# Kernel tuning notes

Measured on AMD Instinct MI355X. Metric: run time of the kernel, lower is better.

The kernel has to match this reference:

```python
import jax, jax.numpy as jnp
from jax import lax
import numpy as np

ROI = 7  # roi_size


def _extract_rois(feat, coords):
    """Faithful port of extract_roi_features: clamp a 7x7 window to image bounds,
    then bilinearly resize the (possibly smaller) crop back to 7x7
    (F.interpolate, mode='bilinear', align_corners=False)."""
    B, C, H, W = feat.shape
    half = ROI // 2

    def axis_idx(c, size):
        start = jnp.maximum(0, c - half)                  # [B,A]
        end = jnp.minimum(size, c + half + 1)
        Li = end - start                                  # crop length (int) [B,A]
        L = Li.astype(feat.dtype)[..., None]              # [B,A,1]
        j = jnp.arange(ROI, dtype=feat.dtype)
        # align_corners=False source coordinate, clamped into the crop
        src = jnp.clip((j + 0.5) * L / ROI - 0.5, 0.0, L - 1.0)  # [B,A,7]
        i0 = jnp.floor(src).astype(jnp.int32)
        i1 = jnp.minimum(i0 + 1, Li[..., None] - 1)
        w1 = src - i0.astype(feat.dtype)
        return start[..., None] + i0, start[..., None] + i1, 1.0 - w1, w1

    xc = coords[..., 0].astype(jnp.int32)
    yc = coords[..., 1].astype(jnp.int32)
    y0, y1, wy0, wy1 = axis_idx(yc, H)
    x0, x1, wx0, wx1 = axis_idx(xc, W)
    Bn, A = xc.shape
    bi = jnp.arange(Bn)[:, None, None, None]

    def g(Y, X):  # gather -> [B,A,7,7,C]
        return feat[bi, :, Y[:, :, :, None], X[:, :, None, :]]

    wy0 = wy0[:, :, :, None, None]; wy1 = wy1[:, :, :, None, None]
    wx0 = wx0[:, :, None, :, None]; wx1 = wx1[:, :, None, :, None]
    v = (wy0 * wx0 * g(y0, x0) + wy0 * wx1 * g(y0, x1)
         + wy1 * wx0 * g(y1, x0) + wy1 * wx1 * g(y1, x1))
    return jnp.transpose(v, (0, 1, 4, 2, 3))  # [B,A,C,7,7]


def _conv(x, w, b, pad):
    y = lax.conv_general_dilated(x, w, (1, 1), [(pad, pad), (pad, pad)],
                                 dimension_numbers=('NCHW', 'OIHW', 'NCHW'))
    return y + b[None, :, None, None]


def _bn(x, scale, bias, mean, var, eps=1e-5):
    inv = scale * lax.rsqrt(var + eps)
    return x * inv[None, :, None, None] + (bias - mean * inv)[None, :, None, None]


def setup_inputs() -> dict:
    key = jax.random.key(0)
    ks = jax.random.split(key, 12)
    B, A, C, H, W = 8, 128, 256, 64, 64
    f32 = jnp.float32
    d = {}
    d['feat_rgb'] = jax.random.normal(ks[0], (B, C, H, W), f32)
    d['feat_tir'] = jax.random.normal(ks[1], (B, C, H, W), f32)
    d['anchor_coords'] = jax.random.randint(ks[2], (B, A, 2), 0, 64).astype(jnp.int32)
    # local_fusion: Conv(2C->C,3) BN ReLU Conv(C->C,3) BN ReLU
    d['conv1_w'] = jax.random.normal(ks[3], (C, 2 * C, 3, 3), f32) * 0.02
    d['conv1_b'] = jnp.zeros((C,), f32)
    d['bn1_scale'] = jnp.ones((C,), f32)
    d['bn1_bias'] = jnp.zeros((C,), f32)
    d['bn1_mean'] = jax.random.normal(ks[4], (C,), f32) * 0.1
    d['bn1_var'] = jax.random.uniform(ks[5], (C,), f32, 0.5, 1.5)
    d['conv2_w'] = jax.random.normal(ks[6], (C, C, 3, 3), f32) * 0.02
    d['conv2_b'] = jnp.zeros((C,), f32)
    d['bn2_scale'] = jnp.ones((C,), f32)
    d['bn2_bias'] = jnp.zeros((C,), f32)
    d['bn2_mean'] = jax.random.normal(ks[7], (C,), f32) * 0.1
    d['bn2_var'] = jax.random.uniform(ks[8], (C,), f32, 0.5, 1.5)
    # weight_generator: Conv(C->C//4,1) ReLU Conv(C//4->2,1) Softmax(dim=1)
    d['wg1_w'] = jax.random.normal(ks[9], (C // 4, C, 1, 1), f32) * 0.05
    d['wg1_b'] = jnp.zeros((C // 4,), f32)
    d['wg2_w'] = jax.random.normal(ks[10], (2, C // 4, 1, 1), f32) * 0.05
    d['wg2_b'] = jnp.zeros((2,), f32)
    return d


def reference(feat_rgb, feat_tir, anchor_coords,
              conv1_w, conv1_b, bn1_scale, bn1_bias, bn1_mean, bn1_var,
              conv2_w, conv2_b, bn2_scale, bn2_bias, bn2_mean, bn2_var,
              wg1_w, wg1_b, wg2_w, wg2_b):
    B, C, H, W = feat_rgb.shape
    A = anchor_coords.shape[1]
    roi_rgb = _extract_rois(feat_rgb, anchor_coords)  # [B,A,C,7,7]
    roi_tir = _extract_rois(feat_tir, anchor_coords)
    rgb = roi_rgb.reshape(B * A, C, ROI, ROI)
    tir = roi_tir.reshape(B * A, C, ROI, ROI)
    x = jnp.concatenate([rgb, tir], axis=1)           # [B*A, 2C, 7, 7]
    x = jax.nn.relu(_bn(_conv(x, conv1_w, conv1_b, 1), bn1_scale, bn1_bias, bn1_mean, bn1_var))
    x = jax.nn.relu(_bn(_conv(x, conv2_w, conv2_b, 1), bn2_scale, bn2_bias, bn2_mean, bn2_var))
    h = jax.nn.relu(_conv(x, wg1_w, wg1_b, 0))
    w = jax.nn.softmax(_conv(h, wg2_w, wg2_b, 0), axis=1)  # [B*A, 2, 7, 7]
    fused = w[:, 0:1] * rgb + w[:, 1:2] * tir
    return fused.reshape(B, A, C, ROI, ROI)
```

## Files before the change

### kernel.cpp

```cpp
#include <hip/hip_runtime.h>
#include <cstddef>
#include <cstdint>


typedef unsigned int u32;
typedef unsigned short u16;
typedef __attribute__((ext_vector_type(8))) short short8;
typedef __attribute__((ext_vector_type(16))) float float16v;

__device__ __forceinline__ float bf2f(u16 u) {
  u32 x = ((u32)u) << 16;
  return __builtin_bit_cast(float, x);
}
__device__ __forceinline__ u16 f2bf(float f) {
  u32 x = __builtin_bit_cast(u32, f);
  x = x + 0x7fffu + ((x >> 16) & 1u);
  return (u16)(x >> 16);
}
__device__ __forceinline__ void gl_lds16(const void* g, void* l) {
  __builtin_amdgcn_global_load_lds((const __attribute__((address_space(1))) void*)g,
                                   (__attribute__((address_space(3))) void*)l, 16, 0, 0);
}

template <int IC>
__global__ void k_prep_w(const float* __restrict__ w, u16* __restrict__ wt) {
  int i = blockIdx.x * 256 + threadIdx.x;
  if (i >= 9 * 256 * IC) return;
  int e = i & 7;
  int r = i >> 3;
  int oc = r & 255;
  int r2 = r >> 8;
  int oct = r2 % (IC / 8);
  int t = r2 / (IC / 8);
  int ic = oct * 8 + e;
  wt[i] = f2bf(w[((size_t)oc * IC + ic) * 9 + t]);
}

__global__ void k_prep_bn(const float* __restrict__ cb, const float* __restrict__ sc,
                          const float* __restrict__ bi, const float* __restrict__ mn,
                          const float* __restrict__ vr, float* __restrict__ sb) {
  int c = threadIdx.x;
  float inv = sc[c] * rsqrtf(vr[c] + 1e-5f);
  sb[c]       = inv;
  sb[256 + c] = cb[c] * inv + (bi[c] - mn[c] * inv);
}

__global__ __launch_bounds__(256)
void k_roi2(const float* __restrict__ frgb, const float* __restrict__ ftir,
            const int* __restrict__ coords, u16* __restrict__ cat) {
  int ba = blockIdx.x, b = ba >> 7, tid = threadIdx.x;
  __shared__ int   si0[2][7], si1[2][7];
  __shared__ float sw0[2][7], sw1[2][7];
  __shared__ u16 tile[49][514];
  if (tid < 14) {
    int axis = tid / 7;
    int j = tid - axis * 7;
    int c = coords[ba * 2 + (axis == 0 ? 1 : 0)];
    int start = max(0, c - 3);
    int end   = min(64, c + 4);
    int Li = end - start;
    float L = (float)Li;
    float src = ((float)j + 0.5f) * L / 7.0f - 0.5f;
    src = fminf(fmaxf(src, 0.0f), L - 1.0f);
    int i0 = (int)floorf(src);
    int i1 = min(i0 + 1, Li - 1);
    float w1 = src - (float)i0;
    si0[axis][j] = start + i0;
    si1[axis][j] = start + i1;
    sw0[axis][j] = 1.0f - w1;
    sw1[axis][j] = w1;
  }
  __syncthreads();
  const float* fr = frgb + (size_t)b * 256 * 4096;
  const float* ft = ftir + (size_t)b * 256 * 4096;
  for (int idx = tid; idx < 256 * 49; idx += 256) {
    int c = idx / 49, p = idx - c * 49;
    int jy = p / 7, jx = p - (p / 7) * 7;
    int y0 = si0[0][jy], y1 = si1[0][jy];
    int x0 = si0[1][jx], x1 = si1[1][jx];
    float wy0 = sw0[0][jy], wy1 = sw1[0][jy];
    float wx0 = sw0[1][jx], wx1 = sw1[1][jx];
    float a00 = wy0 * wx0, a01 = wy0 * wx1, a10 = wy1 * wx0, a11 = wy1 * wx1;
    const float* fc = fr + (size_t)c * 4096;
    float vr_ = a00 * fc[y0 * 64 + x0] + a01 * fc[y0 * 64 + x1] +
                a10 * fc[y1 * 64 + x0] + a11 * fc[y1 * 64 + x1];
    const float* gc = ft + (size_t)c * 4096;
    float vt_ = a00 * gc[y0 * 64 + x0] + a01 * gc[y0 * 64 + x1] +
                a10 * gc[y1 * 64 + x0] + a11 * gc[y1 * 64 + x1];
    tile[p][c]       = f2bf(vr_);
    tile[p][256 + c] = f2bf(vt_);
  }
  __syncthreads();
  u16* dst = cat + (size_t)ba * 49 * 512;
  for (int o = tid; o < 49 * 512; o += 256) {
    int row = o >> 9, c = o & 511;
    dst[o] = tile[row][c];
  }
}

template <int ICT, bool FIRST>
__global__ __launch_bounds__(512, 4)
void k_conv_mfma(const u16* __restrict__ IN, const u16* __restrict__ WT,
                 const float* __restrict__ sb, u16* __restrict__ OUT) {
  constexpr int NC = ICT / 64;
  constexpr int ROIB = 137 * 128;
  constexpr int BUFB = 2 * ROIB;
  __shared__ __align__(16) u16 lds[2][BUFB / 2];
  const int tid = threadIdx.x;
  const int lane = tid & 63, wv = tid >> 6;
  const int ng = wv & 3, mg = wv >> 2;
  const int l31 = lane & 31, h32 = lane >> 5;
  const int ba2 = blockIdx.x * 2;
  const char* inb = (const char*)IN;

  {
    short8 zz = (short8){0, 0, 0, 0, 0, 0, 0, 0};
    short8* lp = (short8*)&lds[0][0];
    for (int z = tid; z < (2 * BUFB) / 16; z += 512) lp[z] = zz;
  }
  __syncthreads();

  int rg[2];
#pragma unroll
  for (int i = 0; i < 2; ++i) {
    int P = (mg * 2 + i) * 32 + l31;
    if (P > 97) P = 97;
    int roi = (P >= 49) ? 1 : 0;
    int q = P - roi * 49;
    int qy = q / 7, qx = q - (q / 7) * 7;
    rg[i] = roi * 137 + qy * 16 + qx;
  }

  float16v acc[2][2];
#pragma unroll
  for (int i = 0; i < 2; ++i)
#pragma unroll
    for (int f = 0; f < 2; ++f)
#pragma unroll
      for (int e = 0; e < 16; ++e) acc[i][f][e] = 0.0f;

  auto stage = [&](int ch, int buf) {
    for (int s = wv; s < 14; s += 8) {
      int roi = s / 7, qy = s - roi * 7;
      char* dbase = (char*)&lds[buf][0] + roi * ROIB + ((qy + 1) * 16 + 1) * 128;
      if (lane < 56) {
        int r = roi * 137 + (qy + 1) * 16 + 1 + (lane >> 3);
        int cl = ((lane & 7) * 16) ^ ((r & 7) << 4);
        const char* src = inb +
            ((size_t)((ba2 + roi) * 49 + qy * 7 + (lane >> 3))) * (ICT * 2) +
            ch * 128 + cl;
        gl_lds16(src, dbase);
      }
    }
  };

  stage(0, 0);
  __syncthreads();

  const u16* wthr = WT + (size_t)h32 * 2048 + (size_t)(ng * 64 + l31) * 8;

  int cur = 0;
#pragma unroll 1
  for (int ch = 0; ch < NC; ++ch) {
    if (ch + 1 < NC) stage(ch + 1, cur ^ 1);
    const char* lb = (const char*)&lds[cur][0];
    const u16* wch = wthr + (size_t)ch * 8 * 2048;

    short8 wfr[4][2];
#pragma unroll
    for (int jp = 0; jp < 3; ++jp)
#pragma unroll
      for (int f = 0; f < 2; ++f)
        wfr[jp][f] = *(const short8*)(
            wch + (size_t)(jp * 2) * 2048 + f * 256);
#pragma unroll
    for (int j = 0; j < 36; ++j) {
      if (j + 3 < 36) {
        const int jn = j + 3;
#pragma unroll
        for (int f = 0; f < 2; ++f)
          wfr[jn & 3][f] = *(const short8*)(
              wch + (size_t)((jn >> 2) * (ICT / 8) + (jn & 3) * 2) * 2048 + f * 256);
      }
      const int t = j >> 2, kk = j & 3;
      const int toff = (t / 3) * 16 + (t - (t / 3) * 3);
      short8 bfr[2];
#pragma unroll
      for (int i = 0; i < 2; ++i) {
        int r = rg[i] + toff;
        int byt = r * 128 + ((kk * 32 + h32 * 16) ^ ((r & 7) << 4));
        bfr[i] = *(const short8*)(lb + byt);
      }
      __builtin_amdgcn_s_setprio(1);
#pragma unroll
      for (int i = 0; i < 2; ++i)
#pragma unroll
        for (int f = 0; f < 2; ++f)
          acc[i][f] = FIRST
              ? __builtin_amdgcn_mfma_f32_32x32x16_bf16(bfr[i], wfr[j & 3][f],
                                                        acc[i][f], 0, 0, 0)
              : __builtin_amdgcn_mfma_f32_32x32x16_bf16(wfr[j & 3][f], bfr[i],
                                                        acc[i][f], 0, 0, 0);
      __builtin_amdgcn_s_setprio(0);
    }
    __syncthreads();
    cur ^= 1;
  }

  if (FIRST) {
    u16* ob = OUT + (size_t)ba2 * 49 * 256;
#pragma unroll
    for (int f = 0; f < 2; ++f) {
      int oc = ng * 64 + f * 32 + l31;
      float s = sb[oc], bb = sb[256 + oc];
#pragma unroll
      for (int i = 0; i < 2; ++i) {
        int tl = mg * 2 + i;
#pragma unroll
        for (int reg = 0; reg < 16; ++reg) {
          int m = (reg & 3) + 8 * (reg >> 2) + 4 * h32;
          int P = tl * 32 + m;
          if (P < 98) {
            int roi = (P >= 49) ? 1 : 0;
            int q = P - roi * 49;
            ob[((size_t)roi * 49 + q) * 256 + oc] =
                f2bf(fmaxf(acc[i][f][reg] * s + bb, 0.0f));
          }
        }
      }
    }
  } else {
    u16* ob = OUT + (size_t)ba2 * 256 * 49;
#pragma unroll
    for (int i = 0; i < 2; ++i) {
      int tl = mg * 2 + i;
      int P = tl * 32 + l31;
      if (P < 98) {
        int roi = (P >= 49) ? 1 : 0;
        int q = P - roi * 49;
#pragma unroll
        for (int f = 0; f < 2; ++f)
#pragma unroll
          for (int reg = 0; reg < 16; ++reg) {
            int oc = ng * 64 + f * 32 + (reg & 3) + 8 * (reg >> 2) + 4 * h32;
            float s = sb[oc], bb = sb[256 + oc];
            ob[((size_t)roi * 256 + oc) * 49 + q] =
                f2bf(fmaxf(acc[i][f][reg] * s + bb, 0.0f));
          }
      }
    }
  }
}

__global__ __launch_bounds__(256)
void k_head_fuse(const u16* __restrict__ x3, const u16* __restrict__ cat,
                 const float* __restrict__ w1, const float* __restrict__ b1,
                 const float* __restrict__ w2, const float* __restrict__ b2,
                 float* __restrict__ out) {
  int ba  = blockIdx.x;
  int tid = threadIdx.x;
  __shared__ float xs[256 * 49];
  __shared__ float hs[64 * 49];
  __shared__ float ls[2 * 49];
  __shared__ float swx[2 * 49];
  const u16* src = x3 + (size_t)ba * 256 * 49;
  for (int idx = tid; idx < 256 * 49; idx += 256) xs[idx] = bf2f(src[idx]);
  __syncthreads();
  for (int idx = tid; idx < 64 * 49; idx += 256) {
    int oh = idx / 49, p = idx - oh * 49;
    float s = b1[oh];
    const float* wr = w1 + oh * 256;
    for (int ic = 0; ic < 256; ++ic) s += wr[ic] * xs[ic * 49 + p];
    hs[idx] = fmaxf(s, 0.0f);
  }
  __syncthreads();
  if (tid < 98) {
    int chn = tid / 49, p = tid - chn * 49;
    float s = b2[chn];
    const float* wr = w2 + chn * 64;
    for (int k = 0; k < 64; ++k) s += wr[k] * hs[k * 49 + p];
    ls[tid] = s;
  }
  __syncthreads();
  if (tid < 49) {
    float l0 = ls[tid], l1 = ls[49 + tid];
    float m = fmaxf(l0, l1);
    float e0 = expf(l0 - m), e1 = expf(l1 - m);
    float d = e0 + e1;
    swx[tid]      = e0 / d;
    swx[49 + tid] = e1 / d;
  }
  __syncthreads();
  const u16* cr = cat + (size_t)ba * 49 * 512;
  float* o = out + (size_t)ba * 256 * 49;
  for (int idx = tid; idx < 256 * 49; idx += 256) {
    int c = idx / 49, p = idx - (idx / 49) * 49;
    float rgb = bf2f(cr[p * 512 + c]);
    float tir = bf2f(cr[p * 512 + 256 + c]);
    o[idx] = swx[p] * rgb + swx[49 + p] * tir;
  }
}

extern "C" void kernel_launch(void* const* d_in, const int* in_sizes, int n_in,
                              void* d_out, int out_size, void* d_ws, size_t ws_size,
                              hipStream_t stream) {
  const float* feat_rgb = (const float*)d_in[0];
  const float* feat_tir = (const float*)d_in[1];
  const int*   coords   = (const int*)d_in[2];
  const float* conv1_w  = (const float*)d_in[3];
  const float* conv1_b  = (const float*)d_in[4];
  const float* bn1_s    = (const float*)d_in[5];
  const float* bn1_b    = (const float*)d_in[6];
  const float* bn1_m    = (const float*)d_in[7];
  const float* bn1_v    = (const float*)d_in[8];
  const float* conv2_w  = (const float*)d_in[9];
  const float* conv2_b  = (const float*)d_in[10];
  const float* bn2_s    = (const float*)d_in[11];
  const float* bn2_b    = (const float*)d_in[12];
  const float* bn2_m    = (const float*)d_in[13];
  const float* bn2_v    = (const float*)d_in[14];
  const float* wg1_w    = (const float*)d_in[15];
  const float* wg1_b    = (const float*)d_in[16];
  const float* wg2_w    = (const float*)d_in[17];
  const float* wg2_b    = (const float*)d_in[18];
  float* out = (float*)d_out;

  char* base = (char*)d_ws;
  u16*   W1T  = (u16*)(base);
  u16*   W2T  = (u16*)(base + 2359296);
  float* SB1  = (float*)(base + 2359296 + 1179648);
  float* SB2  = (float*)(base + 2359296 + 1179648 + 2048);
  u16*   CAT  = (u16*)(base + 3543040);
  u16*   X2   = (u16*)(base + 3543040 + 51380224);
  u16*   X3   = (u16*)(base + 3543040 + 51380224 + 25690112);

  k_prep_w<512><<<(9 * 256 * 512 + 255) / 256, 256, 0, stream>>>(conv1_w, W1T);
  k_prep_w<256><<<(9 * 256 * 256 + 255) / 256, 256, 0, stream>>>(conv2_w, W2T);
  k_prep_bn<<<1, 256, 0, stream>>>(conv1_b, bn1_s, bn1_b, bn1_m, bn1_v, SB1);
  k_prep_bn<<<1, 256, 0, stream>>>(conv2_b, bn2_s, bn2_b, bn2_m, bn2_v, SB2);
  k_roi2<<<1024, 256, 0, stream>>>(feat_rgb, feat_tir, coords, CAT);
  k_conv_mfma<512, true><<<512, 512, 0, stream>>>(CAT, W1T, SB1, X2);
  k_conv_mfma<256, false><<<512, 512, 0, stream>>>(X2, W2T, SB2, X3);
  k_head_fuse<<<1024, 256, 0, stream>>>(X3, CAT, wg1_w, wg1_b, wg2_w, wg2_b, out);
}
```

Measured before the change: 640.2 us.

## Prefetch LDS operand fragments, change swizzle, and use non-temporal LDS loads

The conv MFMA loop now double-buffers the LDS activation fragments, loading iteration j+1 before issuing the MFMAs for j. To balance register use, weight-fragment prefetch depth drops from 3 to 2 buffers. The LDS XOR swizzle now mixes in higher row bits (r ^ r>>4) to reduce bank conflicts, and the global-to-LDS loads use a non-temporal cache policy. Together these aim to hide LDS latency behind the MFMAs. The shallower weight prefetch and the changed cache hint could expose global-load latency.

```diff
diff --git a/kernel.cpp b/kernel.cpp
--- a/kernel.cpp
+++ b/kernel.cpp
@@ -17,9 +17,9 @@
   x = x + 0x7fffu + ((x >> 16) & 1u);
   return (u16)(x >> 16);
 }
-__device__ __forceinline__ void gl_lds16(const void* g, void* l) {
+__device__ __forceinline__ void gl_lds16_nt(const void* g, void* l) {
   __builtin_amdgcn_global_load_lds((const __attribute__((address_space(1))) void*)g,
-                                   (__attribute__((address_space(3))) void*)l, 16, 0, 0);
+                                   (__attribute__((address_space(3))) void*)l, 16, 0, 2);
 }
 
 template <int IC>
@@ -145,11 +145,12 @@
       char* dbase = (char*)&lds[buf][0] + roi * ROIB + ((qy + 1) * 16 + 1) * 128;
       if (lane < 56) {
         int r = roi * 137 + (qy + 1) * 16 + 1 + (lane >> 3);
-        int cl = ((lane & 7) * 16) ^ ((r & 7) << 4);
+        int sw = ((r ^ (r >> 4)) & 7) << 4;
+        int cl = ((lane & 7) * 16) ^ sw;
         const char* src = inb +
             ((size_t)((ba2 + roi) * 49 + qy * 7 + (lane >> 3))) * (ICT * 2) +
             ch * 128 + cl;
-        gl_lds16(src, dbase);
+        gl_lds16_nt(src, dbase);
       }
     }
   };
@@ -166,30 +167,40 @@
     const char* lb = (const char*)&lds[cur][0];
     const u16* wch = wthr + (size_t)ch * 8 * 2048;
 
-    short8 wfr[4][2];
-#pragma unroll
-    for (int jp = 0; jp < 3; ++jp)
+    short8 wfr[3][2];
+#pragma unroll
+    for (int jp = 0; jp < 2; ++jp)
 #pragma unroll
       for (int f = 0; f < 2; ++f)
         wfr[jp][f] = *(const short8*)(
             wch + (size_t)(jp * 2) * 2048 + f * 256);
+    short8 bfr[2][2];
+#pragma unroll
+    for (int i = 0; i < 2; ++i) {
+      int r = rg[i];
+      int byt = r * 128 + ((h32 * 16) ^ (((r ^ (r >> 4)) & 7) << 4));
+      bfr[0][i] = *(const short8*)(lb + byt);
+    }
 #pragma unroll
     for (int j = 0; j < 36; ++j) {
-      if (j + 3 < 36) {
-        const int jn = j + 3;
+      if (j + 2 < 36) {
+        const int jn = j + 2;
 #pragma unroll
         for (int f = 0; f < 2; ++f)
-          wfr[jn & 3][f] = *(const short8*)(
+          wfr[jn % 3][f] = *(const short8*)(
               wch + (size_t)((jn >> 2) * (ICT / 8) + (jn & 3) * 2) * 2048 + f * 256);
       }
-      const int t = j >> 2, kk = j & 3;
-      const int toff = (t / 3) * 16 + (t - (t / 3) * 3);
-      short8 bfr[2];
-#pragma unroll
-      for (int i = 0; i < 2; ++i) {
-        int r = rg[i] + toff;
-        int byt = r * 128 + ((kk * 32 + h32 * 16) ^ ((r & 7) << 4));
-        bfr[i] = *(const short8*)(lb + byt);
+      if (j + 1 < 36) {
+        const int jn = j + 1;
+        const int t2 = jn >> 2, kk2 = jn & 3;
+        const int toff2 = (t2 / 3) * 16 + (t2 - (t2 / 3) * 3);
+#pragma unroll
+        for (int i = 0; i < 2; ++i) {
+          int r = rg[i] + toff2;
+          int byt = r * 128 +
+                    ((kk2 * 32 + h32 * 16) ^ (((r ^ (r >> 4)) & 7) << 4));
+          bfr[jn & 1][i] = *(const short8*)(lb + byt);
+        }
       }
       __builtin_amdgcn_s_setprio(1);
 #pragma unroll
@@ -197,9 +208,9 @@
 #pragma unroll
         for (int f = 0; f < 2; ++f)
           acc[i][f] = FIRST
-              ? __builtin_amdgcn_mfma_f32_32x32x16_bf16(bfr[i], wfr[j & 3][f],
+              ? __builtin_amdgcn_mfma_f32_32x32x16_bf16(bfr[j & 1][i], wfr[j % 3][f],
                                                         acc[i][f], 0, 0, 0)
-              : __builtin_amdgcn_mfma_f32_32x32x16_bf16(wfr[j & 3][f], bfr[i],
+              : __builtin_amdgcn_mfma_f32_32x32x16_bf16(wfr[j % 3][f], bfr[j & 1][i],
                                                         acc[i][f], 0, 0, 0);
       __builtin_amdgcn_s_setprio(0);
     }
```

Result: no change. 632.2 us (-1.3%).

## Process four ROIs per conv block with 1024 threads and compact LDS layout

Applied to the files above, without the earlier changes.

The conv kernel now handles four ROIs per block using 16 waves, so each weight fragment loaded from global memory is reused across twice as many output positions. The padded 16-wide LDS halo layout is replaced by a compact 196-row layout plus one zero row. Out-of-bounds 3x3 taps are redirected to that zero row with a per-tap bounds check, which shrinks staging and LDS zero-fill. Padding waste drops from 128 to 98 positions per ROI pair, with one idle wave group handled via a dead flag. The cost is index arithmetic per tap, fewer blocks (256) for the GPU's many CUs, and higher register pressure at 1024 threads.

```diff
diff --git a/kernel.cpp b/kernel.cpp
--- a/kernel.cpp
+++ b/kernel.cpp
@@ -99,36 +99,37 @@
 }
 
 template <int ICT, bool FIRST>
-__global__ __launch_bounds__(512, 4)
+__global__ __launch_bounds__(1024, 4)
 void k_conv_mfma(const u16* __restrict__ IN, const u16* __restrict__ WT,
                  const float* __restrict__ sb, u16* __restrict__ OUT) {
   constexpr int NC = ICT / 64;
-  constexpr int ROIB = 137 * 128;
-  constexpr int BUFB = 2 * ROIB;
+  constexpr int BUFB = 200 * 128;
   __shared__ __align__(16) u16 lds[2][BUFB / 2];
   const int tid = threadIdx.x;
   const int lane = tid & 63, wv = tid >> 6;
   const int ng = wv & 3, mg = wv >> 2;
   const int l31 = lane & 31, h32 = lane >> 5;
-  const int ba2 = blockIdx.x * 2;
+  const int ba4 = blockIdx.x * 4;
   const char* inb = (const char*)IN;
-
-  {
+  const bool dead1 = (mg == 3);
+
+  if (tid < 64) {
     short8 zz = (short8){0, 0, 0, 0, 0, 0, 0, 0};
-    short8* lp = (short8*)&lds[0][0];
-    for (int z = tid; z < (2 * BUFB) / 16; z += 512) lp[z] = zz;
-  }
-  __syncthreads();
-
-  int rg[2];
+    int buf = tid >> 5, idx = tid & 31;
+    *(short8*)((char*)&lds[buf][0] + 196 * 128 + idx * 16) = zz;
+  }
+  __syncthreads();
+
+  int base_[2], qy_[2], qx_[2];
 #pragma unroll
   for (int i = 0; i < 2; ++i) {
-    int P = (mg * 2 + i) * 32 + l31;
-    if (P > 97) P = 97;
-    int roi = (P >= 49) ? 1 : 0;
+    int P = (mg + 4 * i) * 32 + l31;
+    if (P > 195) P = 195;
+    int roi = P / 49;
     int q = P - roi * 49;
-    int qy = q / 7, qx = q - (q / 7) * 7;
-    rg[i] = roi * 137 + qy * 16 + qx;
+    base_[i] = roi * 49;
+    qy_[i] = q / 7;
+    qx_[i] = q - (q / 7) * 7;
   }
 
   float16v acc[2][2];
@@ -140,16 +141,12 @@
       for (int e = 0; e < 16; ++e) acc[i][f][e] = 0.0f;
 
   auto stage = [&](int ch, int buf) {
-    for (int s = wv; s < 14; s += 8) {
-      int roi = s / 7, qy = s - roi * 7;
-      char* dbase = (char*)&lds[buf][0] + roi * ROIB + ((qy + 1) * 16 + 1) * 128;
-      if (lane < 56) {
-        int r = roi * 137 + (qy + 1) * 16 + 1 + (lane >> 3);
-        int cl = ((lane & 7) * 16) ^ ((r & 7) << 4);
+    int cl = ((lane & 7) * 16) ^ (((lane >> 3) & 7) << 4);
+    for (int s = wv; s < 25; s += 16) {
+      if (s < 24 || lane < 32) {
         const char* src = inb +
-            ((size_t)((ba2 + roi) * 49 + qy * 7 + (lane >> 3))) * (ICT * 2) +
-            ch * 128 + cl;
-        gl_lds16(src, dbase);
+            ((size_t)(ba4 * 49 + s * 8 + (lane >> 3))) * (ICT * 2) + ch * 128 + cl;
+        gl_lds16(src, (char*)&lds[buf][0] + s * 1024);
       }
     }
   };
@@ -166,41 +163,55 @@
     const char* lb = (const char*)&lds[cur][0];
     const u16* wch = wthr + (size_t)ch * 8 * 2048;
 
-    short8 wfr[4][2];
-#pragma unroll
-    for (int jp = 0; jp < 3; ++jp)
+    short8 wfr[3][2];
+#pragma unroll
+    for (int jp = 0; jp < 2; ++jp)
 #pragma unroll
       for (int f = 0; f < 2; ++f)
         wfr[jp][f] = *(const short8*)(
             wch + (size_t)(jp * 2) * 2048 + f * 256);
+    int row0 = 0, row1 = 0;
 #pragma unroll
     for (int j = 0; j < 36; ++j) {
-      if (j + 3 < 36) {
-        const int jn = j + 3;
+      const int t = j >> 2, kk = j & 3;
+      if (kk == 0) {
+        const int dy = t / 3 - 1, dx = t - (t / 3) * 3 - 1;
+#pragma unroll
+        for (int i = 0; i < 2; ++i) {
+          int iy = qy_[i] + dy, ix = qx_[i] + dx;
+          int ok = ((u32)iy < 7u) & ((u32)ix < 7u);
+          int row = ok ? (base_[i] + iy * 7 + ix) : 196;
+          if (i == 0) row0 = row; else row1 = row;
+        }
+      }
+      if (j + 2 < 36) {
+        const int jn = j + 2;
 #pragma unroll
         for (int f = 0; f < 2; ++f)
-          wfr[jn & 3][f] = *(const short8*)(
+          wfr[jn % 3][f] = *(const short8*)(
               wch + (size_t)((jn >> 2) * (ICT / 8) + (jn & 3) * 2) * 2048 + f * 256);
       }
-      const int t = j >> 2, kk = j & 3;
-      const int toff = (t / 3) * 16 + (t - (t / 3) * 3);
       short8 bfr[2];
+      {
+        int byt0 = row0 * 128 + ((kk * 32 + h32 * 16) ^ ((row0 & 7) << 4));
+        bfr[0] = *(const short8*)(lb + byt0);
+      }
+      if (!dead1) {
+        int byt1 = row1 * 128 + ((kk * 32 + h32 * 16) ^ ((row1 & 7) << 4));
+        bfr[1] = *(const short8*)(lb + byt1);
+      }
+      __builtin_amdgcn_s_setprio(1);
 #pragma unroll
       for (int i = 0; i < 2; ++i) {
-        int r = rg[i] + toff;
-        int byt = r * 128 + ((kk * 32 + h32 * 16) ^ ((r & 7) << 4));
-        bfr[i] = *(const short8*)(lb + byt);
-      }
-      __builtin_amdgcn_s_setprio(1);
-#pragma unroll
-      for (int i = 0; i < 2; ++i)
+        if (i == 1 && dead1) continue;
 #pragma unroll
         for (int f = 0; f < 2; ++f)
           acc[i][f] = FIRST
-              ? __builtin_amdgcn_mfma_f32_32x32x16_bf16(bfr[i], wfr[j & 3][f],
+              ? __builtin_amdgcn_mfma_f32_32x32x16_bf16(bfr[i], wfr[j % 3][f],
                                                         acc[i][f], 0, 0, 0)
-              : __builtin_amdgcn_mfma_f32_32x32x16_bf16(wfr[j & 3][f], bfr[i],
+              : __builtin_amdgcn_mfma_f32_32x32x16_bf16(wfr[j % 3][f], bfr[i],
                                                         acc[i][f], 0, 0, 0);
+      }
       __builtin_amdgcn_s_setprio(0);
     }
     __syncthreads();
@@ -208,44 +219,41 @@
   }
 
   if (FIRST) {
-    u16* ob = OUT + (size_t)ba2 * 49 * 256;
+    u16* ob = OUT + (size_t)ba4 * 49 * 256;
 #pragma unroll
     for (int f = 0; f < 2; ++f) {
       int oc = ng * 64 + f * 32 + l31;
       float s = sb[oc], bb = sb[256 + oc];
 #pragma unroll
       for (int i = 0; i < 2; ++i) {
-        int tl = mg * 2 + i;
+        if (i == 1 && dead1) continue;
+        int ti = mg + 4 * i;
 #pragma unroll
         for (int reg = 0; reg < 16; ++reg) {
           int m = (reg & 3) + 8 * (reg >> 2) + 4 * h32;
-          int P = tl * 32 + m;
-          if (P < 98) {
-            int roi = (P >= 49) ? 1 : 0;
-            int q = P - roi * 49;
-            ob[((size_t)roi * 49 + q) * 256 + oc] =
-                f2bf(fmaxf(acc[i][f][reg] * s + bb, 0.0f));
-          }
+          int P = ti * 32 + m;
+          if (P < 196)
+            ob[(size_t)P * 256 + oc] = f2bf(fmaxf(acc[i][f][reg] * s + bb, 0.0f));
         }
       }
     }
   } else {
-    u16* ob = OUT + (size_t)ba2 * 256 * 49;
 #pragma unroll
     for (int i = 0; i < 2; ++i) {
-      int tl = mg * 2 + i;
-      int P = tl * 32 + l31;
-      if (P < 98) {
-        int roi = (P >= 49) ? 1 : 0;
+      if (i == 1 && dead1) continue;
+      int ti = mg + 4 * i;
+      int P = ti * 32 + l31;
+      if (P < 196) {
+        int roi = P / 49;
         int q = P - roi * 49;
+        u16* ob = OUT + ((size_t)(ba4 + roi) * 256) * 49 + q;
 #pragma unroll
         for (int f = 0; f < 2; ++f)
 #pragma unroll
           for (int reg = 0; reg < 16; ++reg) {
             int oc = ng * 64 + f * 32 + (reg & 3) + 8 * (reg >> 2) + 4 * h32;
             float s = sb[oc], bb = sb[256 + oc];
-            ob[((size_t)roi * 256 + oc) * 49 + q] =
-                f2bf(fmaxf(acc[i][f][reg] * s + bb, 0.0f));
+            ob[(size_t)oc * 49] = f2bf(fmaxf(acc[i][f][reg] * s + bb, 0.0f));
           }
       }
     }
@@ -339,7 +347,7 @@
   k_prep_bn<<<1, 256, 0, stream>>>(conv1_b, bn1_s, bn1_b, bn1_m, bn1_v, SB1);
   k_prep_bn<<<1, 256, 0, stream>>>(conv2_b, bn2_s, bn2_b, bn2_m, bn2_v, SB2);
   k_roi2<<<1024, 256, 0, stream>>>(feat_rgb, feat_tir, coords, CAT);
-  k_conv_mfma<512, true><<<512, 512, 0, stream>>>(CAT, W1T, SB1, X2);
-  k_conv_mfma<256, false><<<512, 512, 0, stream>>>(X2, W2T, SB2, X3);
+  k_conv_mfma<512, true><<<256, 1024, 0, stream>>>(CAT, W1T, SB1, X2);
+  k_conv_mfma<256, false><<<256, 1024, 0, stream>>>(X2, W2T, SB2, X3);
   k_head_fuse<<<1024, 256, 0, stream>>>(X3, CAT, wg1_w, wg1_b, wg2_w, wg2_b, out);
 }
```

Measured after the change: 656.1 us. 2.5% more time.
